# Kernel tuning notes

Measured on AMD Instinct MI355X. Metric: run time of the kernel, lower is better.

The kernel has to match this reference:

```python
import jax, jax.numpy as jnp
import numpy as np

BETA = 0.1
GAMMA = 0.5
LABEL_SMOOTHING = 0.0
IGNORE_INDEX = -100

B, T, H, V = 8, 512, 2048, 32000  # B = 2 * num_pairs (first half chosen, second half rejected)


def setup_inputs() -> dict:
    key = jax.random.key(0)
    k1, k2, k3, k4 = jax.random.split(key, 4)
    lin_weight = jax.random.normal(k1, (V, H), dtype=jnp.float32) * 0.02
    _input = jax.random.normal(k2, (B, T, H), dtype=jnp.float32)
    target = jax.random.randint(k3, (B, T), 0, V, dtype=jnp.int64)
    # sprinkle some ignore_index positions like padded labels
    pad = jax.random.uniform(k4, (B, T)) < 0.1
    target = jnp.where(pad, IGNORE_INDEX, target)
    bias = jax.random.normal(k4, (V,), dtype=jnp.float32) * 0.02
    return {"lin_weight": lin_weight, "_input": _input, "target": target, "bias": bias}


def reference(lin_weight, _input, target, bias):
    # fused linear -> log_softmax over vocab
    logits = jnp.einsum("bth,vh->btv", _input, lin_weight) + bias  # (B, T, V)
    logps = jax.nn.log_softmax(logits.astype(jnp.float32), axis=-1)
    # gather target log-probs, masking ignore_index
    mask = (target != IGNORE_INDEX)
    tgt = jnp.where(mask, target, 0)
    per_token_logps = jnp.take_along_axis(logps, tgt[..., None], axis=-1)[..., 0]
    per_token_logps = per_token_logps * mask  # (B, T)
    # SimPO uses length-normalized (average) sequence log-prob
    avg_logps = per_token_logps.sum(-1) / jnp.maximum(mask.sum(-1), 1)  # (B,)
    n_pairs = B // 2
    chosen_logps = avg_logps[:n_pairs]
    rejected_logps = avg_logps[n_pairs:]
    d = BETA * (chosen_logps - rejected_logps) - GAMMA
    loss = (-jax.nn.log_sigmoid(d) * (1.0 - LABEL_SMOOTHING)
            - jax.nn.log_sigmoid(-d) * LABEL_SMOOTHING).sum() / n_pairs
    return loss
```

## Files before the change

kernel.cpp:

```cpp
#include <hip/hip_runtime.h>
#include <stdint.h>
#include <math.h>

constexpr int Bb = 8, Tt = 512, Hh = 2048, Vv = 32000;
constexpr int M = Bb * Tt;
constexpr int K = Hh;
constexpr int N = Vv;
constexpr int NB = N / 128;
constexpr int IGNORE = -100;

typedef __attribute__((ext_vector_type(8))) short bf16x8;
typedef __attribute__((ext_vector_type(4))) float f32x4;

__device__ inline void gld16(const void* g, const void* l) {
  __builtin_amdgcn_global_load_lds(
      (const __attribute__((address_space(1))) uint32_t*)g,
      (__attribute__((address_space(3))) uint32_t*)l, 16, 0, 0);
}

__device__ inline unsigned short f2bf(float f) {
  union { float f; unsigned u; } x; x.f = f;
  unsigned r = x.u + 0x7fffu + ((x.u >> 16) & 1u);
  return (unsigned short)(r >> 16);
}

__global__ void cast_bf16_kernel(const float* __restrict__ src,
                                 unsigned short* __restrict__ dst, int n4) {
  int i = blockIdx.x * blockDim.x + threadIdx.x;
  int stride = gridDim.x * blockDim.x;
  const float4* s4 = (const float4*)src;
  ushort4* d4 = (ushort4*)dst;
  for (; i < n4; i += stride) {
    float4 v = s4[i];
    ushort4 o;
    o.x = f2bf(v.x); o.y = f2bf(v.y); o.z = f2bf(v.z); o.w = f2bf(v.w);
    d4[i] = o;
  }
}

__global__ __launch_bounds__(256)
void gemm_stats(const unsigned short* __restrict__ X,
                const unsigned short* __restrict__ W,
                const float* __restrict__ bias,
                const int* __restrict__ tgt,
                float* __restrict__ m_part,
                float* __restrict__ s_part,
                float* __restrict__ tlogit) {
  __shared__ __align__(16) unsigned short As[128 * 64];
  __shared__ __align__(16) unsigned short Bs[128 * 64];
  __shared__ float red_m[2][128];
  __shared__ float red_s[2][128];

  const int tid = threadIdx.x;
  const int lane = tid & 63;
  const int wid = tid >> 6;
  const int waveM = wid >> 1;
  const int waveN = wid & 1;
  const int q = lane >> 4;
  const int c = lane & 15;
  const int bm = blockIdx.x;
  const int bn = blockIdx.y;

  const int srow = lane >> 3;
  const int scol = ((lane & 7) ^ srow) * 8;
  const unsigned short* gA = X + (size_t)(bm * 128 + wid * 32 + srow) * K + scol;
  const unsigned short* gB = W + (size_t)(bn * 128 + wid * 32 + srow) * K + scol;

  f32x4 acc[4][4];
#pragma unroll
  for (int i = 0; i < 4; ++i)
#pragma unroll
    for (int j = 0; j < 4; ++j) acc[i][j] = (f32x4){0.f, 0.f, 0.f, 0.f};

  for (int k0 = 0; k0 < K; k0 += 64) {
#pragma unroll
    for (int j = 0; j < 4; ++j) {
      gld16(gA + (size_t)j * 8 * K + k0, As + (wid * 32 + j * 8) * 64);
      gld16(gB + (size_t)j * 8 * K + k0, Bs + (wid * 32 + j * 8) * 64);
    }
    __syncthreads();
#pragma unroll
    for (int kk = 0; kk < 2; ++kk) {
      bf16x8 af[4], bfr[4];
#pragma unroll
      for (int i = 0; i < 4; ++i) {
        const int rA = waveM * 64 + i * 16 + c;
        const int rB = waveN * 64 + i * 16 + c;
        const int chunk = kk * 4 + q;
        af[i]  = *(const bf16x8*)(As + rA * 64 + ((chunk ^ (rA & 7)) * 8));
        bfr[i] = *(const bf16x8*)(Bs + rB * 64 + ((chunk ^ (rB & 7)) * 8));
      }
#pragma unroll
      for (int mi = 0; mi < 4; ++mi)
#pragma unroll
        for (int ni = 0; ni < 4; ++ni)
          acc[mi][ni] = __builtin_amdgcn_mfma_f32_16x16x32_bf16(
              af[mi], bfr[ni], acc[mi][ni], 0, 0, 0);
    }
    __syncthreads();
  }

  const int colBase = bn * 128 + waveN * 64;
  float bvals[4];
#pragma unroll
  for (int ni = 0; ni < 4; ++ni) bvals[ni] = bias[colBase + ni * 16 + c];

#pragma unroll
  for (int mi = 0; mi < 4; ++mi) {
    const int rowBase = bm * 128 + waveM * 64 + mi * 16 + q * 4;
#pragma unroll
    for (int reg = 0; reg < 4; ++reg) {
      const int grow = rowBase + reg;
      const int t = tgt[grow];
      float v[4];
      float mloc = -3.4e38f;
#pragma unroll
      for (int ni = 0; ni < 4; ++ni) {
        v[ni] = acc[mi][ni][reg] + bvals[ni];
        mloc = fmaxf(mloc, v[ni]);
        const int gn = colBase + ni * 16 + c;
        if (gn == t) tlogit[grow] = v[ni];
      }
#pragma unroll
      for (int off = 1; off < 16; off <<= 1) mloc = fmaxf(mloc, __shfl_xor(mloc, off));
      float sloc = 0.f;
#pragma unroll
      for (int ni = 0; ni < 4; ++ni) sloc += __expf(v[ni] - mloc);
#pragma unroll
      for (int off = 1; off < 16; off <<= 1) sloc += __shfl_xor(sloc, off);
      if (c == 0) {
        const int lrow = waveM * 64 + mi * 16 + q * 4 + reg;
        red_m[waveN][lrow] = mloc;
        red_s[waveN][lrow] = sloc;
      }
    }
  }
  __syncthreads();
  if (tid < 128) {
    const float m0 = red_m[0][tid], m1 = red_m[1][tid];
    const float s0 = red_s[0][tid], s1 = red_s[1][tid];
    const float mx = fmaxf(m0, m1);
    const float ss = s0 * __expf(m0 - mx) + s1 * __expf(m1 - mx);
    const int grow = bm * 128 + tid;
    m_part[(size_t)grow * NB + bn] = mx;
    s_part[(size_t)grow * NB + bn] = ss;
  }
}

__global__ __launch_bounds__(256)
void combine_rows(const float* __restrict__ m_part, const float* __restrict__ s_part,
                  const float* __restrict__ tlogit, const int* __restrict__ tgt,
                  float* __restrict__ logp) {
  const int row = blockIdx.x * 4 + (threadIdx.x >> 6);
  const int lane = threadIdx.x & 63;
  const float* mrow = m_part + (size_t)row * NB;
  const float* srow = s_part + (size_t)row * NB;
  float mv[4], sv[4];
  int cnt = 0;
  float mx = -3.4e38f;
  for (int cc = lane; cc < NB; cc += 64) {
    mv[cnt] = mrow[cc]; sv[cnt] = srow[cc];
    mx = fmaxf(mx, mv[cnt]); ++cnt;
  }
#pragma unroll
  for (int off = 32; off >= 1; off >>= 1) mx = fmaxf(mx, __shfl_xor(mx, off));
  float s = 0.f;
  for (int i = 0; i < cnt; ++i) s += sv[i] * __expf(mv[i] - mx);
#pragma unroll
  for (int off = 32; off >= 1; off >>= 1) s += __shfl_xor(s, off);
  if (lane == 0) {
    const int t = tgt[row];
    logp[row] = (t == IGNORE) ? 0.f : (tlogit[row] - mx - logf(s));
  }
}

__global__ void finalize(const float* __restrict__ logp, const int* __restrict__ tgt,
                         float* __restrict__ out) {
  __shared__ float avg[8];
  const int w = threadIdx.x >> 6;
  const int lane = threadIdx.x & 63;
  float s = 0.f, cnt = 0.f;
  for (int i = lane; i < Tt; i += 64) {
    const int idx = w * Tt + i;
    s += logp[idx];
    cnt += (tgt[idx] != IGNORE) ? 1.f : 0.f;
  }
#pragma unroll
  for (int off = 32; off >= 1; off >>= 1) {
    s += __shfl_xor(s, off);
    cnt += __shfl_xor(cnt, off);
  }
  if (lane == 0) avg[w] = s / fmaxf(cnt, 1.f);
  __syncthreads();
  if (threadIdx.x == 0) {
    float loss = 0.f;
#pragma unroll
    for (int p = 0; p < 4; ++p) {
      const float d = 0.1f * (avg[p] - avg[p + 4]) - 0.5f;
      const float nl = (d > 0.f) ? log1pf(expf(-d)) : (-d + log1pf(expf(d)));
      loss += nl;
    }
    out[0] = loss * 0.25f;
  }
}

extern "C" void kernel_launch(void* const* d_in, const int* in_sizes, int n_in,
                              void* d_out, int out_size, void* d_ws, size_t ws_size,
                              hipStream_t stream) {
  const float* Wf   = (const float*)d_in[0];
  const float* Xf   = (const float*)d_in[1];
  const int*   tgt  = (const int*)d_in[2];
  const float* bias = (const float*)d_in[3];
  float* out = (float*)d_out;

  char* ws = (char*)d_ws;
  size_t off = 0;
  auto alloc = [&](size_t bytes) {
    void* p = ws + off;
    off += (bytes + 255) & ~(size_t)255;
    return p;
  };
  unsigned short* Xbf = (unsigned short*)alloc((size_t)M * K * 2);
  unsigned short* Wbf = (unsigned short*)alloc((size_t)N * K * 2);
  float* m_part = (float*)alloc((size_t)M * NB * 4);
  float* s_part = (float*)alloc((size_t)M * NB * 4);
  float* tlog   = (float*)alloc((size_t)M * 4);
  float* logp   = (float*)alloc((size_t)M * 4);

  cast_bf16_kernel<<<2048, 256, 0, stream>>>(Xf, Xbf, M * K / 4);
  cast_bf16_kernel<<<8192, 256, 0, stream>>>(Wf, Wbf, N * K / 4);

  dim3 grid(M / 128, NB);
  gemm_stats<<<grid, 256, 0, stream>>>(Xbf, Wbf, bias, tgt, m_part, s_part, tlog);

  combine_rows<<<M / 4, 256, 0, stream>>>(m_part, s_part, tlog, tgt, logp);
  finalize<<<1, 512, 0, stream>>>(logp, tgt, out);
}
```

Measured before the change: 1.063 ms.

## Double-buffer LDS tiles in GEMM to overlap global loads with MFMA

```diff
diff --git a/kernel.cpp b/kernel.cpp
--- a/kernel.cpp
+++ b/kernel.cpp
@@ -7,6 +7,7 @@
 constexpr int K = Hh;
 constexpr int N = Vv;
 constexpr int NB = N / 128;
+constexpr int KITERS = K / 64;
 constexpr int IGNORE = -100;
 
 typedef __attribute__((ext_vector_type(8))) short bf16x8;
@@ -46,8 +47,10 @@
                 float* __restrict__ m_part,
                 float* __restrict__ s_part,
                 float* __restrict__ tlogit) {
-  __shared__ __align__(16) unsigned short As[128 * 64];
-  __shared__ __align__(16) unsigned short Bs[128 * 64];
+  __shared__ __align__(16) unsigned short As0[128 * 64];
+  __shared__ __align__(16) unsigned short As1[128 * 64];
+  __shared__ __align__(16) unsigned short Bs0[128 * 64];
+  __shared__ __align__(16) unsigned short Bs1[128 * 64];
   __shared__ float red_m[2][128];
   __shared__ float red_s[2][128];
 
@@ -65,6 +68,19 @@
   const int scol = ((lane & 7) ^ srow) * 8;
   const unsigned short* gA = X + (size_t)(bm * 128 + wid * 32 + srow) * K + scol;
   const unsigned short* gB = W + (size_t)(bn * 128 + wid * 32 + srow) * K + scol;
+  const int ldsRow = wid * 32 + srow;
+
+  int offA[2][4], offB[2][4];
+#pragma unroll
+  for (int kk = 0; kk < 2; ++kk)
+#pragma unroll
+    for (int i = 0; i < 4; ++i) {
+      const int rA = waveM * 64 + i * 16 + c;
+      const int rB = waveN * 64 + i * 16 + c;
+      const int chunk = kk * 4 + q;
+      offA[kk][i] = rA * 64 + ((chunk ^ (rA & 7)) * 8);
+      offB[kk][i] = rB * 64 + ((chunk ^ (rB & 7)) * 8);
+    }
 
   f32x4 acc[4][4];
 #pragma unroll
@@ -72,23 +88,22 @@
 #pragma unroll
     for (int j = 0; j < 4; ++j) acc[i][j] = (f32x4){0.f, 0.f, 0.f, 0.f};
 
-  for (int k0 = 0; k0 < K; k0 += 64) {
+  auto stage = [&](unsigned short* Ad, unsigned short* Bd, int tile) {
+    const size_t k0 = (size_t)tile * 64;
 #pragma unroll
     for (int j = 0; j < 4; ++j) {
-      gld16(gA + (size_t)j * 8 * K + k0, As + (wid * 32 + j * 8) * 64);
-      gld16(gB + (size_t)j * 8 * K + k0, Bs + (wid * 32 + j * 8) * 64);
-    }
-    __syncthreads();
+      gld16(gA + (size_t)j * 8 * K + k0, Ad + (ldsRow + j * 8) * 64);
+      gld16(gB + (size_t)j * 8 * K + k0, Bd + (ldsRow + j * 8) * 64);
+    }
+  };
+  auto compute = [&](const unsigned short* Asb, const unsigned short* Bsb) {
 #pragma unroll
     for (int kk = 0; kk < 2; ++kk) {
       bf16x8 af[4], bfr[4];
 #pragma unroll
       for (int i = 0; i < 4; ++i) {
-        const int rA = waveM * 64 + i * 16 + c;
-        const int rB = waveN * 64 + i * 16 + c;
-        const int chunk = kk * 4 + q;
-        af[i]  = *(const bf16x8*)(As + rA * 64 + ((chunk ^ (rA & 7)) * 8));
-        bfr[i] = *(const bf16x8*)(Bs + rB * 64 + ((chunk ^ (rB & 7)) * 8));
+        af[i]  = *(const bf16x8*)(Asb + offA[kk][i]);
+        bfr[i] = *(const bf16x8*)(Bsb + offB[kk][i]);
       }
 #pragma unroll
       for (int mi = 0; mi < 4; ++mi)
@@ -97,8 +112,23 @@
           acc[mi][ni] = __builtin_amdgcn_mfma_f32_16x16x32_bf16(
               af[mi], bfr[ni], acc[mi][ni], 0, 0, 0);
     }
+  };
+
+  stage(As0, Bs0, 0);
+
+  for (int i2 = 0; i2 < KITERS / 2 - 1; ++i2) {
     __syncthreads();
-  }
+    stage(As1, Bs1, 2 * i2 + 1);
+    compute(As0, Bs0);
+    __syncthreads();
+    stage(As0, Bs0, 2 * i2 + 2);
+    compute(As1, Bs1);
+  }
+  __syncthreads();
+  stage(As1, Bs1, KITERS - 1);
+  compute(As0, Bs0);
+  __syncthreads();
+  compute(As1, Bs1);
 
   const int colBase = bn * 128 + waveN * 64;
   float bvals[4];
```

Result: no change. 1.042 ms (-2.0%).
